# Optimization experiments

Measured on AMD Instinct MI355X. Metric: run time of the kernel, lower is better.

The kernel has to match this reference:

```python
import jax, jax.numpy as jnp
import numpy as np

N = 50000
E = 1200000
IN_DIM = 128
HID = 16      # out_channels of conv1 per head
HEADS1 = 8
OUT_DIM = 128  # conv2 out_channels, heads=1
EPS = 1e-16


def _linear_params(key, fan_in, fan_out):
    kw, kb = jax.random.split(key)
    s = 1.0 / np.sqrt(fan_in)
    W = jax.random.uniform(kw, (fan_in, fan_out), minval=-s, maxval=s, dtype=jnp.float32)
    b = jax.random.uniform(kb, (fan_out,), minval=-s, maxval=s, dtype=jnp.float32)
    return W, b


def setup_inputs() -> dict:
    key = jax.random.key(0)
    ks = jax.random.split(key, 10)
    x = jax.random.normal(ks[0], (N, IN_DIM), dtype=jnp.float32)
    edge_index = jax.random.randint(ks[1], (2, E), 0, N, dtype=jnp.int64)
    # conv1: in=128, heads=8, per-head=16 -> H*C = 128
    Wq1, bq1 = _linear_params(ks[2], IN_DIM, HEADS1 * HID)
    Wk1, bk1 = _linear_params(ks[3], IN_DIM, HEADS1 * HID)
    Wv1, bv1 = _linear_params(ks[4], IN_DIM, HEADS1 * HID)
    Ws1, bs1 = _linear_params(ks[5], IN_DIM, HEADS1 * HID)
    # conv2: in=128, heads=1, per-head=OUT_DIM
    Wq2, bq2 = _linear_params(ks[6], HEADS1 * HID, OUT_DIM)
    Wk2, bk2 = _linear_params(ks[7], HEADS1 * HID, OUT_DIM)
    Wv2, bv2 = _linear_params(ks[8], HEADS1 * HID, OUT_DIM)
    Ws2, bs2 = _linear_params(ks[9], HEADS1 * HID, OUT_DIM)
    return dict(x=x, edge_index=edge_index,
                Wq1=Wq1, bq1=bq1, Wk1=Wk1, bk1=bk1, Wv1=Wv1, bv1=bv1, Ws1=Ws1, bs1=bs1,
                Wq2=Wq2, bq2=bq2, Wk2=Wk2, bk2=bk2, Wv2=Wv2, bv2=bv2, Ws2=Ws2, bs2=bs2)


def _transformer_conv(x, src, dst, Wq, bq, Wk, bk, Wv, bv, Ws, bs, heads, ch):
    """PyG TransformerConv (concat=True, root_weight=True, no edge_attr)."""
    n = x.shape[0]
    q = (x @ Wq + bq).reshape(n, heads, ch)
    k = (x @ Wk + bk).reshape(n, heads, ch)
    v = (x @ Wv + bv).reshape(n, heads, ch)
    # per-edge attention logits: message from src j to dst i
    alpha = jnp.einsum('ehc,ehc->eh', q[dst], k[src]) / np.sqrt(ch)  # [E, H]
    # segment softmax over incoming edges of each destination node
    m = jax.ops.segment_max(alpha, dst, num_segments=n)              # [N, H]
    m = jnp.where(jnp.isfinite(m), m, 0.0)
    ea = jnp.exp(alpha - jax.lax.stop_gradient(m)[dst])
    denom = jax.ops.segment_sum(ea, dst, num_segments=n)             # [N, H]
    attn = ea / (denom[dst] + EPS)                                   # [E, H]
    out = jax.ops.segment_sum(attn[:, :, None] * v[src], dst, num_segments=n)  # [N, H, C]
    return out.reshape(n, heads * ch) + (x @ Ws + bs)                # skip (root) connection


def reference(x, edge_index,
              Wq1, bq1, Wk1, bk1, Wv1, bv1, Ws1, bs1,
              Wq2, bq2, Wk2, bk2, Wv2, bv2, Ws2, bs2):
    src, dst = edge_index[0], edge_index[1]
    h = _transformer_conv(x, src, dst, Wq1, bq1, Wk1, bk1, Wv1, bv1, Ws1, bs1, HEADS1, HID)
    out = _transformer_conv(h, src, dst, Wq2, bq2, Wk2, bk2, Wv2, bv2, Ws2, bs2, 1, OUT_DIM)
    return out
```

## Files before the change

kernel.cpp:

```cpp
#include <hip/hip_runtime.h>
#include <cstdint>

#define N_NODES 50000
#define N_EDGES 1200000
#define NP2 50176
#define NSCAN 196
#define BM 64
#define GT 782
#define NWG 1564

typedef __attribute__((ext_vector_type(8))) short short8;
typedef __attribute__((ext_vector_type(4))) float f32x4;

__device__ __forceinline__ unsigned short f2bf(float x) {
    unsigned u = __float_as_uint(x);
    unsigned r = (u + 0x7FFFu + ((u >> 16) & 1u)) >> 16;
    return (unsigned short)r;
}
__device__ __forceinline__ float bf2f(unsigned short h) {
    return __uint_as_float(((unsigned)h) << 16);
}
__device__ __forceinline__ int swz(int row, int kbyte) {
    return row * 256 + (kbyte ^ ((row & 7) << 4));
}

__global__ __launch_bounds__(256) void prep_w(
    const float* __restrict__ W0, const float* __restrict__ W1,
    const float* __restrict__ W2, const float* __restrict__ W3,
    const float* __restrict__ W4, const float* __restrict__ W5,
    const float* __restrict__ W6, const float* __restrict__ W7,
    unsigned short* __restrict__ WTH)
{
    int g = blockIdx.x * 256 + threadIdx.x;
    int m = g >> 14, o = g & 16383;
    int n = o >> 7, k = o & 127;
    const float* W;
    switch (m) {
        case 0: W = W0; break; case 1: W = W1; break;
        case 2: W = W2; break; case 3: W = W3; break;
        case 4: W = W4; break; case 5: W = W5; break;
        case 6: W = W6; break; default: W = W7; break;
    }
    WTH[g] = f2bf(W[k * 128 + n]);
}

__global__ __launch_bounds__(256, 2) void gemm_mfma(
    const float* __restrict__ A, int nrows,
    const unsigned short* __restrict__ WT,
    const float* __restrict__ b0, const float* __restrict__ b1,
    const float* __restrict__ b2, const float* __restrict__ b3,
    float* __restrict__ O0, unsigned short* __restrict__ O1,
    unsigned short* __restrict__ O2, float* __restrict__ O3)
{
    __shared__ unsigned short As[BM * 128];
    __shared__ unsigned short Bs[2 * 128 * 128];

    const int orig = blockIdx.x;
    const int xcd = orig & 7, lid = orig >> 3;
    const int wgid = ((xcd < 4) ? xcd * 196 : 784 + (xcd - 4) * 195) + lid;
    const int xt = wgid >> 1;
    const int p  = wgid & 1;
    const int row0 = xt * BM;
    const int t = threadIdx.x;

    #pragma unroll
    for (int i = 0; i < 4; ++i) {
        int chunk = t + i * 256;
        int row = chunk >> 4, c8 = chunk & 15;
        int gr = row0 + row;
        float4 a0, a1;
        if (gr < nrows) {
            a0 = *(const float4*)(A + (size_t)gr * 128 + c8 * 8);
            a1 = *(const float4*)(A + (size_t)gr * 128 + c8 * 8 + 4);
        } else {
            a0 = make_float4(0.f, 0.f, 0.f, 0.f);
            a1 = a0;
        }
        short8 h;
        h[0] = f2bf(a0.x); h[1] = f2bf(a0.y); h[2] = f2bf(a0.z); h[3] = f2bf(a0.w);
        h[4] = f2bf(a1.x); h[5] = f2bf(a1.y); h[6] = f2bf(a1.z); h[7] = f2bf(a1.w);
        *(short8*)((char*)As + swz(row, c8 * 16)) = h;
    }
    #pragma unroll
    for (int i = 0; i < 16; ++i) {
        int chunk = t + i * 256;
        int o = chunk >> 11, n = (chunk >> 4) & 127, c8 = chunk & 15;
        short8 b = *(const short8*)(WT + ((size_t)(p * 2 + o) * 16384 + n * 128 + c8 * 8));
        *(short8*)((char*)Bs + o * 32768 + swz(n, c8 * 16)) = b;
    }
    __syncthreads();

    const int lane = t & 63;
    const int w    = t >> 6;
    const int o    = w & 1;
    const int rg2  = w >> 1;
    const int mi   = lane & 15;
    const int kg   = lane >> 4;

    f32x4 acc[2][8] = {};

    #pragma unroll
    for (int ks = 0; ks < 4; ++ks) {
        const int kb = ks * 64 + kg * 16;
        short8 a0 = *(const short8*)((char*)As + swz(rg2 * 32 + mi, kb));
        short8 a1 = *(const short8*)((char*)As + swz(rg2 * 32 + 16 + mi, kb));
        #pragma unroll
        for (int ct = 0; ct < 8; ++ct) {
            short8 b = *(const short8*)((char*)Bs + o * 32768 + swz(ct * 16 + mi, kb));
            acc[0][ct] = __builtin_amdgcn_mfma_f32_16x16x32_bf16(a0, b, acc[0][ct], 0, 0, 0);
            acc[1][ct] = __builtin_amdgcn_mfma_f32_16x16x32_bf16(a1, b, acc[1][ct], 0, 0, 0);
        }
    }

    const int out = p * 2 + o;
    const float* bptr = (out == 0) ? b0 : (out == 1) ? b1 : (out == 2) ? b2 : b3;
    const int g2 = lane >> 4;
    #pragma unroll
    for (int ct = 0; ct < 8; ++ct) {
        int col = ct * 16 + mi;
        float bias_v = bptr[col];
        #pragma unroll
        for (int tile = 0; tile < 2; ++tile) {
            #pragma unroll
            for (int r = 0; r < 4; ++r) {
                int grow = row0 + rg2 * 32 + tile * 16 + g2 * 4 + r;
                if (grow < nrows) {
                    float val = acc[tile][ct][r] + bias_v;
                    size_t idx = (size_t)grow * 128 + col;
                    if (out == 0)      O0[idx] = val;
                    else if (out == 1) O1[idx] = f2bf(val);
                    else if (out == 2) O2[idx] = f2bf(val);
                    else               O3[idx] = val;
                }
            }
        }
    }
}

__global__ __launch_bounds__(256) void hist_k(const int* __restrict__ dst, int* __restrict__ deg)
{
    int e = blockIdx.x * 256 + threadIdx.x;
    if (e >= N_EDGES) return;
    atomicAdd(&deg[dst[e]], 1);
}

__global__ __launch_bounds__(256) void scan1_k(const int* __restrict__ deg, int* __restrict__ bsum)
{
    __shared__ int s[256];
    int t = threadIdx.x;
    s[t] = deg[blockIdx.x * 256 + t];
    __syncthreads();
    for (int off = 128; off > 0; off >>= 1) {
        if (t < off) s[t] += s[t + off];
        __syncthreads();
    }
    if (t == 0) bsum[blockIdx.x] = s[0];
}

__global__ __launch_bounds__(256) void scan2_k(const int* __restrict__ bsum, int* __restrict__ boff,
                                               int* __restrict__ rowptr)
{
    __shared__ int s[256];
    int t = threadIdx.x;
    int v = (t < NSCAN) ? bsum[t] : 0;
    s[t] = v;
    __syncthreads();
    for (int off = 1; off < 256; off <<= 1) {
        int v2 = (t >= off) ? s[t - off] : 0;
        __syncthreads();
        s[t] += v2;
        __syncthreads();
    }
    if (t < NSCAN) boff[t] = s[t] - v;
    if (t == 0) rowptr[N_NODES] = N_EDGES;
}

__global__ __launch_bounds__(256) void scan3_k(const int* __restrict__ deg, const int* __restrict__ boff,
                                               int* __restrict__ rowptr, int* __restrict__ cursor)
{
    __shared__ int s[256];
    int t = threadIdx.x;
    int i = blockIdx.x * 256 + t;
    int d = deg[i];
    s[t] = d;
    __syncthreads();
    for (int off = 1; off < 256; off <<= 1) {
        int v2 = (t >= off) ? s[t - off] : 0;
        __syncthreads();
        s[t] += v2;
        __syncthreads();
    }
    if (i < N_NODES) {
        int val = boff[blockIdx.x] + s[t] - d;
        rowptr[i] = val;
        cursor[i] = val;
    }
}

__global__ __launch_bounds__(256) void fill_k(
    const int* __restrict__ src, const int* __restrict__ dst,
    int* __restrict__ cursor, int* __restrict__ esrc)
{
    int e = blockIdx.x * 256 + threadIdx.x;
    if (e >= N_EDGES) return;
    int p = atomicAdd(&cursor[dst[e]], 1);
    esrc[p] = src[e];
}

template<int H>
__global__ __launch_bounds__(256) void fused_attn(
    const float* __restrict__ Qm, const unsigned short* __restrict__ Km,
    const unsigned short* __restrict__ Vm, const float* __restrict__ Sm,
    const int* __restrict__ rowptr, const int* __restrict__ esrc,
    float* __restrict__ out, float scale)
{
    const int n = blockIdx.x * 4 + (threadIdx.x >> 6);
    const int l = threadIdx.x & 63;
    const int i = l >> 3;
    const int h = l & 7;
    const int start = rowptr[n];
    const int cnt   = rowptr[n + 1] - start;

    float q[16];
    {
        const float4* qp = (const float4*)(Qm + (size_t)n * 128 + h * 16);
        #pragma unroll
        for (int r = 0; r < 4; ++r) {
            float4 v = qp[r];
            q[4*r+0] = v.x * scale; q[4*r+1] = v.y * scale;
            q[4*r+2] = v.z * scale; q[4*r+3] = v.w * scale;
        }
    }

    float acc[16];
    #pragma unroll
    for (int c = 0; c < 16; ++c) acc[c] = 0.f;
    float den = 0.f;

    for (int base = 0; base < cnt; base += 8) {
        const int ei = base + i;
        const bool valid = ei < cnt;
        const int s = esrc[start + (valid ? ei : 0)];
        const short8* kp = (const short8*)(Km + (size_t)s * 128 + h * 16);
        short8 k0 = kp[0], k1 = kp[1];
        const short8* vp = (const short8*)(Vm + (size_t)s * 128 + h * 16);
        short8 v0 = vp[0], v1 = vp[1];

        float d0 = 0.f, d1 = 0.f;
        #pragma unroll
        for (int c = 0; c < 8; ++c) {
            d0 += bf2f((unsigned short)k0[c]) * q[c];
            d1 += bf2f((unsigned short)k1[c]) * q[8 + c];
        }
        float d = d0 + d1;
        if (H == 1) {
            d += __shfl_xor(d, 1);
            d += __shfl_xor(d, 2);
            d += __shfl_xor(d, 4);
        }
        float ea = valid ? __expf(d) : 0.f;
        den += ea;
        #pragma unroll
        for (int c = 0; c < 8; ++c) {
            acc[c]     += ea * bf2f((unsigned short)v0[c]);
            acc[8 + c] += ea * bf2f((unsigned short)v1[c]);
        }
    }

    #pragma unroll
    for (int m = 8; m <= 32; m <<= 1) {
        den += __shfl_xor(den, m);
        #pragma unroll
        for (int c = 0; c < 16; ++c) acc[c] += __shfl_xor(acc[c], m);
    }

    if (l < 8) {
        float rd = 1.f / (den + 1e-16f);
        const float4* sp = (const float4*)(Sm + (size_t)n * 128 + l * 16);
        float4*       op = (float4*)(out + (size_t)n * 128 + l * 16);
        #pragma unroll
        for (int r = 0; r < 4; ++r) {
            float4 sv = sp[r];
            float4 ov;
            ov.x = acc[4*r+0] * rd + sv.x;
            ov.y = acc[4*r+1] * rd + sv.y;
            ov.z = acc[4*r+2] * rd + sv.z;
            ov.w = acc[4*r+3] * rd + sv.w;
            op[r] = ov;
        }
    }
}

extern "C" void kernel_launch(void* const* d_in, const int* in_sizes, int n_in,
                              void* d_out, int out_size, void* d_ws, size_t ws_size,
                              hipStream_t stream)
{
    const float* x       = (const float*)d_in[0];
    const int*   ei      = (const int*)d_in[1];
    const int*   esrc_in = ei;
    const int*   edst_in = ei + N_EDGES;

    const float* Wq1 = (const float*)d_in[2];  const float* bq1 = (const float*)d_in[3];
    const float* Wk1 = (const float*)d_in[4];  const float* bk1 = (const float*)d_in[5];
    const float* Wv1 = (const float*)d_in[6];  const float* bv1 = (const float*)d_in[7];
    const float* Ws1 = (const float*)d_in[8];  const float* bs1 = (const float*)d_in[9];
    const float* Wq2 = (const float*)d_in[10]; const float* bq2 = (const float*)d_in[11];
    const float* Wk2 = (const float*)d_in[12]; const float* bk2 = (const float*)d_in[13];
    const float* Wv2 = (const float*)d_in[14]; const float* bv2 = (const float*)d_in[15];
    const float* Ws2 = (const float*)d_in[16]; const float* bs2 = (const float*)d_in[17];

    float* out = (float*)d_out;

    char* base = (char*)d_ws;
    const size_t NF4 = (size_t)N_NODES * 128 * 4;
    const size_t NF2 = (size_t)N_NODES * 128 * 2;
    size_t off = 0;
    float*          Q    = (float*)(base + off);          off += NF4;
    float*          S    = (float*)(base + off);          off += NF4;
    unsigned short* Kb   = (unsigned short*)(base + off); off += NF2;
    unsigned short* Vb   = (unsigned short*)(base + off); off += NF2;
    unsigned short* WTH  = (unsigned short*)(base + off); off += 8 * 16384 * 2;
    int*            DEG  = (int*)(base + off);            off += (size_t)NP2 * 4;
    int*            ROW  = (int*)(base + off);            off += (size_t)NP2 * 4;
    int*            CUR  = (int*)(base + off);            off += (size_t)NP2 * 4;
    int*            BSUM = (int*)(base + off);            off += 1024;
    int*            BOFF = (int*)(base + off);            off += 1024;
    int*            ESRC = (int*)(base + off);            off += (size_t)N_EDGES * 4;
    if (ws_size < off) return;

    const int EB1 = (N_EDGES + 255) / 256;
    const int FB  = N_NODES / 4;

    hipMemsetAsync(DEG, 0, (size_t)NP2 * 4, stream);

    prep_w<<<512, 256, 0, stream>>>(Wq1, Wk1, Wv1, Ws1, Wq2, Wk2, Wv2, Ws2, WTH);

    hist_k<<<EB1, 256, 0, stream>>>(edst_in, DEG);
    scan1_k<<<NSCAN, 256, 0, stream>>>(DEG, BSUM);
    scan2_k<<<1, 256, 0, stream>>>(BSUM, BOFF, ROW);
    scan3_k<<<NSCAN, 256, 0, stream>>>(DEG, BOFF, ROW, CUR);
    fill_k<<<EB1, 256, 0, stream>>>(esrc_in, edst_in, CUR, ESRC);

    gemm_mfma<<<NWG, 256, 0, stream>>>(x, N_NODES, WTH,
        bq1, bk1, bv1, bs1, Q, Kb, Vb, S);
    fused_attn<8><<<FB, 256, 0, stream>>>(Q, Kb, Vb, S, ROW, ESRC, out, 0.25f);

    gemm_mfma<<<NWG, 256, 0, stream>>>(out, N_NODES, WTH + 4 * 16384,
        bq2, bk2, bv2, bs2, Q, Kb, Vb, S);
    fused_attn<1><<<FB, 256, 0, stream>>>(Q, Kb, Vb, S, ROW, ESRC, out, 0.08838834764831845f);
}
```

Before: 551.6 us.

## Replace global-atomic CSR fill with two-pass bucketed fill using LDS atomics

The single-pass CSR fill, which used a global atomicAdd per edge on a cursor array, becomes two passes. First, edges are binned by destination into 25 coarse buckets of 2048 nodes, with per-block LDS histograms reserving space in a staging buffer. Second, one workgroup per bucket places edges using LDS cursors. This trades many contended global atomics for an extra 8-byte-per-edge staging write and read. The second pass runs only 25 workgroups, which badly underuses the GPU.

```diff
diff --git a/kernel.cpp b/kernel.cpp
--- a/kernel.cpp
+++ b/kernel.cpp
@@ -6,8 +6,9 @@
 #define NP2 50176
 #define NSCAN 196
 #define BM 64
-#define GT 782
 #define NWG 1564
+#define NB 25
+#define BCAP 52224
 
 typedef __attribute__((ext_vector_type(8))) short short8;
 typedef __attribute__((ext_vector_type(4))) float f32x4;
@@ -176,7 +177,7 @@
 }
 
 __global__ __launch_bounds__(256) void scan3_k(const int* __restrict__ deg, const int* __restrict__ boff,
-                                               int* __restrict__ rowptr, int* __restrict__ cursor)
+                                               int* __restrict__ rowptr)
 {
     __shared__ int s[256];
     int t = threadIdx.x;
@@ -190,21 +191,56 @@
         s[t] += v2;
         __syncthreads();
     }
-    if (i < N_NODES) {
-        int val = boff[blockIdx.x] + s[t] - d;
-        rowptr[i] = val;
-        cursor[i] = val;
-    }
-}
-
-__global__ __launch_bounds__(256) void fill_k(
+    if (i < N_NODES) rowptr[i] = boff[blockIdx.x] + s[t] - d;
+}
+
+__global__ __launch_bounds__(32) void init_tails(int* __restrict__ tail)
+{
+    int t = threadIdx.x;
+    if (t < NB) tail[t] = t * BCAP;
+}
+
+__global__ __launch_bounds__(256) void bucket1(
     const int* __restrict__ src, const int* __restrict__ dst,
-    int* __restrict__ cursor, int* __restrict__ esrc)
-{
-    int e = blockIdx.x * 256 + threadIdx.x;
-    if (e >= N_EDGES) return;
-    int p = atomicAdd(&cursor[dst[e]], 1);
-    esrc[p] = src[e];
+    int* __restrict__ tail, int2* __restrict__ ebuf)
+{
+    __shared__ int hist[NB];
+    __shared__ int base[NB];
+    const int t = threadIdx.x;
+    const int e = blockIdx.x * 256 + t;
+    if (t < NB) hist[t] = 0;
+    __syncthreads();
+    int b = 0, myoff = 0, s = 0, d = 0;
+    const bool valid = e < N_EDGES;
+    if (valid) {
+        s = src[e]; d = dst[e];
+        b = d >> 11;
+        myoff = atomicAdd(&hist[b], 1);
+    }
+    __syncthreads();
+    if (t < NB && hist[t] > 0) base[t] = atomicAdd(&tail[t], hist[t]);
+    __syncthreads();
+    if (valid) ebuf[base[b] + myoff] = make_int2(s, d);
+}
+
+__global__ __launch_bounds__(256) void bucket2(
+    const int2* __restrict__ ebuf, const int* __restrict__ tail,
+    const int* __restrict__ rowptr, int* __restrict__ esrc)
+{
+    __shared__ int cur[2048];
+    const int b = blockIdx.x;
+    const int t = threadIdx.x;
+    const int node0 = b << 11;
+    #pragma unroll
+    for (int i = t; i < 2048; i += 256)
+        cur[i] = (node0 + i < N_NODES) ? rowptr[node0 + i] : 0;
+    __syncthreads();
+    const int cnt = tail[b] - b * BCAP;
+    for (int e = t; e < cnt; e += 256) {
+        int2 ed = ebuf[b * BCAP + e];
+        int p = atomicAdd(&cur[ed.y - node0], 1);
+        esrc[p] = ed.x;
+    }
 }
 
 template<int H>
@@ -322,10 +358,11 @@
     unsigned short* WTH  = (unsigned short*)(base + off); off += 8 * 16384 * 2;
     int*            DEG  = (int*)(base + off);            off += (size_t)NP2 * 4;
     int*            ROW  = (int*)(base + off);            off += (size_t)NP2 * 4;
-    int*            CUR  = (int*)(base + off);            off += (size_t)NP2 * 4;
     int*            BSUM = (int*)(base + off);            off += 1024;
     int*            BOFF = (int*)(base + off);            off += 1024;
+    int*            TAIL = (int*)(base + off);            off += 256;
     int*            ESRC = (int*)(base + off);            off += (size_t)N_EDGES * 4;
+    int2*           EBUF = (int2*)(base + off);           off += (size_t)NB * BCAP * 8;
     if (ws_size < off) return;
 
     const int EB1 = (N_EDGES + 255) / 256;
@@ -335,11 +372,13 @@
 
     prep_w<<<512, 256, 0, stream>>>(Wq1, Wk1, Wv1, Ws1, Wq2, Wk2, Wv2, Ws2, WTH);
 
+    init_tails<<<1, 32, 0, stream>>>(TAIL);
     hist_k<<<EB1, 256, 0, stream>>>(edst_in, DEG);
+    bucket1<<<EB1, 256, 0, stream>>>(esrc_in, edst_in, TAIL, EBUF);
     scan1_k<<<NSCAN, 256, 0, stream>>>(DEG, BSUM);
     scan2_k<<<1, 256, 0, stream>>>(BSUM, BOFF, ROW);
-    scan3_k<<<NSCAN, 256, 0, stream>>>(DEG, BOFF, ROW, CUR);
-    fill_k<<<EB1, 256, 0, stream>>>(esrc_in, edst_in, CUR, ESRC);
+    scan3_k<<<NSCAN, 256, 0, stream>>>(DEG, BOFF, ROW);
+    bucket2<<<NB, 256, 0, stream>>>(EBUF, TAIL, ROW, ESRC);
 
     gemm_mfma<<<NWG, 256, 0, stream>>>(x, N_NODES, WTH,
         bq1, bk1, bv1, bs1, Q, Kb, Vb, S);
```

After: 595.1 us. +7.9%, slower.
